# Kernel optimization log

Hardware: AMD Instinct MI355X
Metric: run time of the kernel (lower is better)

## Reference

```python
import jax, jax.numpy as jnp
import numpy as np

WH, WW, WD = 4, 4, 4
NUM_HEADS = 12


def _relative_coords():
    # (3, N) flattened coords of the 3D window, N = WH*WW*WD
    g = jnp.stack(jnp.meshgrid(jnp.arange(WH), jnp.arange(WW), jnp.arange(WD), indexing='ij'), axis=0)
    flat = g.reshape(3, -1)
    rel = flat[:, :, None] - flat[:, None, :]          # (3, N, N)
    return jnp.transpose(rel, (1, 2, 0)).astype(jnp.float32)  # (N, N, 3)


def setup_inputs() -> dict:
    key = jax.random.key(0)
    ks = jax.random.split(key, 9)
    B_, N, C = 2048, WH * WW * WD, 384
    s = lambda fan: 1.0 / np.sqrt(fan)
    return {
        'x': jax.random.normal(ks[0], (B_, N, C), jnp.float32),
        'qkv_w': jax.random.normal(ks[1], (C, 3 * C), jnp.float32) * s(C),
        'qkv_b': jax.random.normal(ks[2], (3 * C,), jnp.float32) * 0.02,
        'proj_w': jax.random.normal(ks[3], (C, C), jnp.float32) * s(C),
        'proj_b': jax.random.normal(ks[4], (C,), jnp.float32) * 0.02,
        'mlp_w1': jax.random.normal(ks[5], (3, 64), jnp.float32) * s(3),
        'mlp_b1': jax.random.normal(ks[6], (64,), jnp.float32) * 0.02,
        'mlp_w2': jax.random.normal(ks[7], (64, NUM_HEADS), jnp.float32) * s(64),
        'mlp_b2': jax.random.normal(ks[8], (NUM_HEADS,), jnp.float32) * 0.02,
    }


def reference(x, qkv_w, qkv_b, proj_w, proj_b, mlp_w1, mlp_b1, mlp_w2, mlp_b2):
    B_, N, C = x.shape
    H = NUM_HEADS
    hd = C // H
    scale = hd ** -0.5

    qkv = (x @ qkv_w + qkv_b).reshape(B_, N, 3, H, hd)
    q, k, v = qkv[:, :, 0], qkv[:, :, 1], qkv[:, :, 2]   # (B_, N, H, hd)

    # MLP-based relative position bias: (N, N, 3) -> (H, N, N)
    rel = _relative_coords()
    bias = jax.nn.relu(rel @ mlp_w1 + mlp_b1) @ mlp_w2 + mlp_b2  # (N, N, H)
    bias = jnp.transpose(bias, (2, 0, 1))                        # (H, N, N)

    attn = jnp.einsum('bnhd,bmhd->bhnm', q, k) * scale + bias[None]
    attn = jax.nn.softmax(attn, axis=-1)

    out = jnp.einsum('bhnm,bmhd->bnhd', attn, v).reshape(B_, N, C)
    return out @ proj_w + proj_b
```

## Files before the change

kernel.cpp:

```cpp
#include <hip/hip_runtime.h>
#include <stdint.h>

#define NTOK 64
#define CDIM 384
#define NH   12
#define HD   32
#define SCALE 0.17677669529663687f

typedef __attribute__((ext_vector_type(8))) short short8;
typedef __attribute__((ext_vector_type(4))) float floatx4;

__device__ __forceinline__ unsigned short f2bf(float f) {
    union { float f; unsigned u; } v; v.f = f;
    unsigned r = (v.u + 0x7fffu + ((v.u >> 16) & 1u)) >> 16;
    return (unsigned short)r;
}

__global__ void prep_weights(const float* __restrict__ qkv_w,
                             const float* __restrict__ proj_w,
                             unsigned short* __restrict__ qkv_wt,
                             unsigned short* __restrict__ proj_wt) {
    int i = blockIdx.x * blockDim.x + threadIdx.x;
    const int nq = 1152 * 384;
    const int np = 384 * 384;
    if (i < nq) {
        int r = i / 384, c = i - r * 384;
        qkv_wt[i] = f2bf(qkv_w[c * 1152 + r]);
    } else if (i < nq + np) {
        int o = i - nq;
        int r = o / 384, c = o - r * 384;
        proj_wt[o] = f2bf(proj_w[c * 384 + r]);
    }
}

__global__ void prep_bias(const float* __restrict__ w1, const float* __restrict__ b1,
                          const float* __restrict__ w2, const float* __restrict__ b2,
                          float* __restrict__ bt) {
    int t = blockIdx.x * blockDim.x + threadIdx.x;
    int i = t >> 6, j = t & 63;
    float r0 = (float)((i >> 4) - (j >> 4));
    float r1 = (float)(((i >> 2) & 3) - ((j >> 2) & 3));
    float r2 = (float)((i & 3) - (j & 3));
    float acc[NH];
#pragma unroll
    for (int h = 0; h < NH; ++h) acc[h] = b2[h];
    for (int u = 0; u < 64; ++u) {
        float hv = r0 * w1[u] + r1 * w1[64 + u] + r2 * w1[128 + u] + b1[u];
        hv = fmaxf(hv, 0.f);
#pragma unroll
        for (int h = 0; h < NH; ++h) acc[h] += hv * w2[u * NH + h];
    }
    for (int h = 0; h < NH; ++h) bt[(h << 12) + (i << 6) + j] = acc[h];
}

#define XP  392
#define QKP 40
#define VTP 72
#define PBP 72

__launch_bounds__(256, 1)
__global__ void win_attn(const float* __restrict__ x,
                         const unsigned short* __restrict__ qkv_wt,
                         const float* __restrict__ qkv_b,
                         const unsigned short* __restrict__ proj_wt,
                         const float* __restrict__ proj_b,
                         const float* __restrict__ bt,
                         float* __restrict__ out) {
    __shared__ unsigned short xs[64 * XP];
    __shared__ unsigned short ao[64 * XP];
    __shared__ unsigned short qls[2][64 * QKP];
    __shared__ unsigned short kls[2][64 * QKP];
    __shared__ unsigned short vts[2][32 * VTP];
    __shared__ unsigned short pbs[2][64 * PBP];
    const int tid  = threadIdx.x;
    const int lane = tid & 63;
    const int w    = tid >> 6;
    const int l15  = lane & 15;
    const int quad = lane >> 4;
    const int b    = blockIdx.x;

    const float* xb = x + (size_t)b * (64 * 384);
    for (int it = 0; it < 24; ++it) {
        int idx = it * 256 + tid;
        int row = idx / 96;
        int c4  = idx - row * 96;
        const float4 v = *reinterpret_cast<const float4*>(xb + row * 384 + c4 * 4);
        uint2 pk;
        pk.x = (unsigned)f2bf(v.x) | ((unsigned)f2bf(v.y) << 16);
        pk.y = (unsigned)f2bf(v.z) | ((unsigned)f2bf(v.w) << 16);
        *reinterpret_cast<uint2*>(&xs[row * XP + c4 * 4]) = pk;
    }
    __syncthreads();

    const int hh = w >> 1;
    const int d2 = w & 1;
    float rs[2][4];
    const floatx4 zf4 = {0.f, 0.f, 0.f, 0.f};

#pragma unroll 1
    for (int hp = 0; hp < 6; ++hp) {
        floatx4 acc[3][4];
#pragma unroll
        for (int j = 0; j < 3; ++j)
#pragma unroll
            for (int m = 0; m < 4; ++m) acc[j][m] = zf4;

        int colbase[3];
#pragma unroll
        for (int j = 0; j < 3; ++j)
            colbase[j] = j * 384 + (2 * hp + hh) * 32 + d2 * 16;

#pragma unroll
        for (int kk = 0; kk < 12; ++kk) {
            short8 a[4];
#pragma unroll
            for (int m = 0; m < 4; ++m)
                a[m] = *reinterpret_cast<const short8*>(
                    &xs[(16 * m + l15) * XP + kk * 32 + quad * 8]);
#pragma unroll
            for (int j = 0; j < 3; ++j) {
                const short8 bf = *reinterpret_cast<const short8*>(
                    qkv_wt + (size_t)(colbase[j] + l15) * 384 + kk * 32 + quad * 8);
#pragma unroll
                for (int m = 0; m < 4; ++m)
                    acc[j][m] = __builtin_amdgcn_mfma_f32_16x16x32_bf16(a[m], bf, acc[j][m], 0, 0, 0);
            }
        }
#pragma unroll
        for (int j = 0; j < 3; ++j) {
            const float bc = qkv_b[colbase[j] + l15];
            if (j < 2) {
                unsigned short* dst = (j == 0) ? qls[hh] : kls[hh];
#pragma unroll
                for (int m = 0; m < 4; ++m)
#pragma unroll
                    for (int r = 0; r < 4; ++r) {
                        int tok = 16 * m + quad * 4 + r;
                        dst[tok * QKP + d2 * 16 + l15] = f2bf(acc[j][m][r] + bc);
                    }
            } else {
#pragma unroll
                for (int m = 0; m < 4; ++m) {
                    uint2 pk;
                    pk.x = (unsigned)f2bf(acc[2][m][0] + bc) | ((unsigned)f2bf(acc[2][m][1] + bc) << 16);
                    pk.y = (unsigned)f2bf(acc[2][m][2] + bc) | ((unsigned)f2bf(acc[2][m][3] + bc) << 16);
                    *reinterpret_cast<uint2*>(
                        &vts[hh][(d2 * 16 + l15) * VTP + 16 * m + quad * 4]) = pk;
                }
            }
        }
        __syncthreads();

#pragma unroll
        for (int hi = 0; hi < 2; ++hi) {
            const int h = 2 * hp + hi;
            const short8 aq = *reinterpret_cast<const short8*>(
                &qls[hi][(16 * w + l15) * QKP + quad * 8]);
            floatx4 s4[4];
#pragma unroll
            for (int c = 0; c < 4; ++c) {
                const short8 bk = *reinterpret_cast<const short8*>(
                    &kls[hi][(16 * c + l15) * QKP + quad * 8]);
                s4[c] = __builtin_amdgcn_mfma_f32_16x16x32_bf16(aq, bk, zf4, 0, 0, 0);
            }
            const float* bth = bt + ((size_t)h << 12);
#pragma unroll
            for (int r = 0; r < 4; ++r) {
                const int n = 16 * w + quad * 4 + r;
#pragma unroll
                for (int c = 0; c < 4; ++c)
                    s4[c][r] = s4[c][r] * SCALE + bth[(n << 6) + 16 * c + l15];
                float m0 = fmaxf(fmaxf(s4[0][r], s4[1][r]), fmaxf(s4[2][r], s4[3][r]));
#pragma unroll
                for (int sh = 1; sh < 16; sh <<= 1) m0 = fmaxf(m0, __shfl_xor(m0, sh, 16));
                float p0 = 0.f;
#pragma unroll
                for (int c = 0; c < 4; ++c) {
                    float p = __expf(s4[c][r] - m0);
                    s4[c][r] = p;
                    p0 += p;
                }
#pragma unroll
                for (int sh = 1; sh < 16; sh <<= 1) p0 += __shfl_xor(p0, sh, 16);
                rs[hi][r] = 1.f / p0;
#pragma unroll
                for (int c = 0; c < 4; ++c)
                    pbs[hi][n * PBP + 16 * c + l15] = f2bf(s4[c][r]);
            }
        }
        __syncthreads();

#pragma unroll
        for (int hi = 0; hi < 2; ++hi) {
            const int h = 2 * hp + hi;
            short8 ap[2];
#pragma unroll
            for (int kk = 0; kk < 2; ++kk)
                ap[kk] = *reinterpret_cast<const short8*>(
                    &pbs[hi][(16 * w + l15) * PBP + kk * 32 + quad * 8]);
#pragma unroll
            for (int t = 0; t < 2; ++t) {
                floatx4 oacc = zf4;
#pragma unroll
                for (int kk = 0; kk < 2; ++kk) {
                    const short8 bv = *reinterpret_cast<const short8*>(
                        &vts[hi][(16 * t + l15) * VTP + kk * 32 + quad * 8]);
                    oacc = __builtin_amdgcn_mfma_f32_16x16x32_bf16(ap[kk], bv, oacc, 0, 0, 0);
                }
#pragma unroll
                for (int r = 0; r < 4; ++r) {
                    int tok = 16 * w + quad * 4 + r;
                    ao[tok * XP + h * 32 + 16 * t + l15] = f2bf(oacc[r] * rs[hi][r]);
                }
            }
        }
        __syncthreads();
    }

    float* ob = out + (size_t)b * (64 * 384);
#pragma unroll 1
    for (int pass = 0; pass < 2; ++pass) {
        const int ntb = pass * 12 + w * 3;
        floatx4 acc2[3][4];
#pragma unroll
        for (int j = 0; j < 3; ++j)
#pragma unroll
            for (int m = 0; m < 4; ++m) acc2[j][m] = zf4;

#pragma unroll
        for (int kk = 0; kk < 12; ++kk) {
            short8 a2[4];
#pragma unroll
            for (int m = 0; m < 4; ++m)
                a2[m] = *reinterpret_cast<const short8*>(
                    &ao[(16 * m + l15) * XP + kk * 32 + quad * 8]);
#pragma unroll
            for (int j = 0; j < 3; ++j) {
                const short8 bf = *reinterpret_cast<const short8*>(
                    proj_wt + (size_t)((ntb + j) * 16 + l15) * 384 + kk * 32 + quad * 8);
#pragma unroll
                for (int m = 0; m < 4; ++m)
                    acc2[j][m] = __builtin_amdgcn_mfma_f32_16x16x32_bf16(a2[m], bf, acc2[j][m], 0, 0, 0);
            }
        }
#pragma unroll
        for (int j = 0; j < 3; ++j) {
            const int col = (ntb + j) * 16 + l15;
            const float pbias = proj_b[col];
#pragma unroll
            for (int m = 0; m < 4; ++m)
#pragma unroll
                for (int r = 0; r < 4; ++r)
                    ob[(16 * m + quad * 4 + r) * 384 + col] = acc2[j][m][r] + pbias;
        }
    }
}

extern "C" void kernel_launch(void* const* d_in, const int* in_sizes, int n_in,
                              void* d_out, int out_size, void* d_ws, size_t ws_size,
                              hipStream_t stream) {
    const float* x      = (const float*)d_in[0];
    const float* qkv_w  = (const float*)d_in[1];
    const float* qkv_b  = (const float*)d_in[2];
    const float* proj_w = (const float*)d_in[3];
    const float* proj_b = (const float*)d_in[4];
    const float* mlp_w1 = (const float*)d_in[5];
    const float* mlp_b1 = (const float*)d_in[6];
    const float* mlp_w2 = (const float*)d_in[7];
    const float* mlp_b2 = (const float*)d_in[8];
    float* out = (float*)d_out;

    unsigned short* qkv_wt  = (unsigned short*)d_ws;
    unsigned short* proj_wt = qkv_wt + 1152 * 384;
    float*          bt      = (float*)(proj_wt + 384 * 384);

    prep_weights<<<2304, 256, 0, stream>>>(qkv_w, proj_w, qkv_wt, proj_wt);
    prep_bias<<<16, 256, 0, stream>>>(mlp_w1, mlp_b1, mlp_w2, mlp_b2, bt);
    win_attn<<<2048, 256, 0, stream>>>(x, qkv_wt, qkv_b, proj_wt, proj_b, bt, out);
}
```

Measured before the change: 874.4 us.

## Double block to 512 threads and split window work across eight waves

Launches the window-attention kernel with 8 wavefronts instead of 4. The QKV GEMM is split by token halves, each wave handles one head's row block in softmax and PV, and the projection is done in one pass. Because each wave only reads back the probability rows it wrote itself, the barrier between softmax and PV is removed. The aim is more latency hiding and fewer barriers, at the cost of halving per-wave MFMA reuse of the global weight fragments. That means more weight loads per block and a tighter register budget under launch_bounds(512,2).

```diff
diff --git a/kernel.cpp b/kernel.cpp
--- a/kernel.cpp
+++ b/kernel.cpp
@@ -58,7 +58,7 @@
 #define VTP 72
 #define PBP 72
 
-__launch_bounds__(256, 1)
+__launch_bounds__(512, 2)
 __global__ void win_attn(const float* __restrict__ x,
                          const unsigned short* __restrict__ qkv_wt,
                          const float* __restrict__ qkv_b,
@@ -80,8 +80,9 @@
     const int b    = blockIdx.x;
 
     const float* xb = x + (size_t)b * (64 * 384);
-    for (int it = 0; it < 24; ++it) {
-        int idx = it * 256 + tid;
+#pragma unroll
+    for (int it = 0; it < 12; ++it) {
+        int idx = it * 512 + tid;
         int row = idx / 96;
         int c4  = idx - row * 96;
         const float4 v = *reinterpret_cast<const float4*>(xb + row * 384 + c4 * 4);
@@ -92,18 +93,22 @@
     }
     __syncthreads();
 
-    const int hh = w >> 1;
-    const int d2 = w & 1;
-    float rs[2][4];
+    const int hh = w & 1;
+    const int d2 = (w >> 1) & 1;
+    const int mh = w >> 2;
+    const int hi = w >> 2;
+    const int rb = w & 3;
+
+    float rs[4];
     const floatx4 zf4 = {0.f, 0.f, 0.f, 0.f};
 
 #pragma unroll 1
     for (int hp = 0; hp < 6; ++hp) {
-        floatx4 acc[3][4];
+        floatx4 acc[3][2];
 #pragma unroll
         for (int j = 0; j < 3; ++j)
 #pragma unroll
-            for (int m = 0; m < 4; ++m) acc[j][m] = zf4;
+            for (int mi = 0; mi < 2; ++mi) acc[j][mi] = zf4;
 
         int colbase[3];
 #pragma unroll
@@ -112,18 +117,18 @@
 
 #pragma unroll
         for (int kk = 0; kk < 12; ++kk) {
-            short8 a[4];
-#pragma unroll
-            for (int m = 0; m < 4; ++m)
-                a[m] = *reinterpret_cast<const short8*>(
-                    &xs[(16 * m + l15) * XP + kk * 32 + quad * 8]);
+            short8 a[2];
+#pragma unroll
+            for (int mi = 0; mi < 2; ++mi)
+                a[mi] = *reinterpret_cast<const short8*>(
+                    &xs[(16 * (2 * mh + mi) + l15) * XP + kk * 32 + quad * 8]);
 #pragma unroll
             for (int j = 0; j < 3; ++j) {
                 const short8 bf = *reinterpret_cast<const short8*>(
                     qkv_wt + (size_t)(colbase[j] + l15) * 384 + kk * 32 + quad * 8);
 #pragma unroll
-                for (int m = 0; m < 4; ++m)
-                    acc[j][m] = __builtin_amdgcn_mfma_f32_16x16x32_bf16(a[m], bf, acc[j][m], 0, 0, 0);
+                for (int mi = 0; mi < 2; ++mi)
+                    acc[j][mi] = __builtin_amdgcn_mfma_f32_16x16x32_bf16(a[mi], bf, acc[j][mi], 0, 0, 0);
             }
         }
 #pragma unroll
@@ -132,30 +137,29 @@
             if (j < 2) {
                 unsigned short* dst = (j == 0) ? qls[hh] : kls[hh];
 #pragma unroll
-                for (int m = 0; m < 4; ++m)
+                for (int mi = 0; mi < 2; ++mi)
 #pragma unroll
                     for (int r = 0; r < 4; ++r) {
-                        int tok = 16 * m + quad * 4 + r;
-                        dst[tok * QKP + d2 * 16 + l15] = f2bf(acc[j][m][r] + bc);
+                        int tok = 16 * (2 * mh + mi) + quad * 4 + r;
+                        dst[tok * QKP + d2 * 16 + l15] = f2bf(acc[j][mi][r] + bc);
                     }
             } else {
 #pragma unroll
-                for (int m = 0; m < 4; ++m) {
+                for (int mi = 0; mi < 2; ++mi) {
                     uint2 pk;
-                    pk.x = (unsigned)f2bf(acc[2][m][0] + bc) | ((unsigned)f2bf(acc[2][m][1] + bc) << 16);
-                    pk.y = (unsigned)f2bf(acc[2][m][2] + bc) | ((unsigned)f2bf(acc[2][m][3] + bc) << 16);
+                    pk.x = (unsigned)f2bf(acc[2][mi][0] + bc) | ((unsigned)f2bf(acc[2][mi][1] + bc) << 16);
+                    pk.y = (unsigned)f2bf(acc[2][mi][2] + bc) | ((unsigned)f2bf(acc[2][mi][3] + bc) << 16);
                     *reinterpret_cast<uint2*>(
-                        &vts[hh][(d2 * 16 + l15) * VTP + 16 * m + quad * 4]) = pk;
+                        &vts[hh][(d2 * 16 + l15) * VTP + 16 * (2 * mh + mi) + quad * 4]) = pk;
                 }
             }
         }
         __syncthreads();
 
-#pragma unroll
-        for (int hi = 0; hi < 2; ++hi) {
+        {
             const int h = 2 * hp + hi;
             const short8 aq = *reinterpret_cast<const short8*>(
-                &qls[hi][(16 * w + l15) * QKP + quad * 8]);
+                &qls[hi][(16 * rb + l15) * QKP + quad * 8]);
             floatx4 s4[4];
 #pragma unroll
             for (int c = 0; c < 4; ++c) {
@@ -166,7 +170,7 @@
             const float* bth = bt + ((size_t)h << 12);
 #pragma unroll
             for (int r = 0; r < 4; ++r) {
-                const int n = 16 * w + quad * 4 + r;
+                const int n = 16 * rb + quad * 4 + r;
 #pragma unroll
                 for (int c = 0; c < 4; ++c)
                     s4[c][r] = s4[c][r] * SCALE + bth[(n << 6) + 16 * c + l15];
@@ -182,22 +186,20 @@
                 }
 #pragma unroll
                 for (int sh = 1; sh < 16; sh <<= 1) p0 += __shfl_xor(p0, sh, 16);
-                rs[hi][r] = 1.f / p0;
+                rs[r] = 1.f / p0;
 #pragma unroll
                 for (int c = 0; c < 4; ++c)
                     pbs[hi][n * PBP + 16 * c + l15] = f2bf(s4[c][r]);
             }
         }
-        __syncthreads();
-
-#pragma unroll
-        for (int hi = 0; hi < 2; ++hi) {
+
+        {
             const int h = 2 * hp + hi;
             short8 ap[2];
 #pragma unroll
             for (int kk = 0; kk < 2; ++kk)
                 ap[kk] = *reinterpret_cast<const short8*>(
-                    &pbs[hi][(16 * w + l15) * PBP + kk * 32 + quad * 8]);
+                    &pbs[hi][(16 * rb + l15) * PBP + kk * 32 + quad * 8]);
 #pragma unroll
             for (int t = 0; t < 2; ++t) {
                 floatx4 oacc = zf4;
@@ -209,8 +211,8 @@
                 }
 #pragma unroll
                 for (int r = 0; r < 4; ++r) {
-                    int tok = 16 * w + quad * 4 + r;
-                    ao[tok * XP + h * 32 + 16 * t + l15] = f2bf(oacc[r] * rs[hi][r]);
+                    int tok = 16 * rb + quad * 4 + r;
+                    ao[tok * XP + h * 32 + 16 * t + l15] = f2bf(oacc[r] * rs[r]);
                 }
             }
         }
@@ -218,9 +220,8 @@
     }
 
     float* ob = out + (size_t)b * (64 * 384);
-#pragma unroll 1
-    for (int pass = 0; pass < 2; ++pass) {
-        const int ntb = pass * 12 + w * 3;
+    {
+        const int ntb = w * 3;
         floatx4 acc2[3][4];
 #pragma unroll
         for (int j = 0; j < 3; ++j)
@@ -276,5 +277,5 @@
 
     prep_weights<<<2304, 256, 0, stream>>>(qkv_w, proj_w, qkv_wt, proj_wt);
     prep_bias<<<16, 256, 0, stream>>>(mlp_w1, mlp_b1, mlp_w2, mlp_b2, bt);
-    win_attn<<<2048, 256, 0, stream>>>(x, qkv_wt, qkv_b, proj_wt, proj_b, bt, out);
-}
+    win_attn<<<2048, 512, 0, stream>>>(x, qkv_wt, qkv_b, proj_wt, proj_b, bt, out);
+}
```

Measured after the change: 918.3 us. 5.0% more time.

## Restructure window attention to 6 waves, per-head loop, fused incremental projection

Applied to the files above, without the earlier changes.

The block grows to 384 threads (6 waves) and processes one head per iteration instead of head pairs: each wave computes one 16-column slice of q, k or v. The attention output for that head goes into a small per-head LDS tile and is immediately accumulated into the output projection in registers, which removes the full 64x384 attention-output LDS buffer. Shared memory drops roughly by half, targeting 3 blocks per CU. The trade-off is more barriers per head, idle waves during softmax (only 4 of 6 active), and a larger persistent register accumulator.

```diff
diff --git a/kernel.cpp b/kernel.cpp
--- a/kernel.cpp
+++ b/kernel.cpp
@@ -1,10 +1,6 @@
 #include <hip/hip_runtime.h>
 #include <stdint.h>
 
-#define NTOK 64
-#define CDIM 384
-#define NH   12
-#define HD   32
 #define SCALE 0.17677669529663687f
 
 typedef __attribute__((ext_vector_type(8))) short short8;
@@ -41,24 +37,25 @@
     float r0 = (float)((i >> 4) - (j >> 4));
     float r1 = (float)(((i >> 2) & 3) - ((j >> 2) & 3));
     float r2 = (float)((i & 3) - (j & 3));
-    float acc[NH];
-#pragma unroll
-    for (int h = 0; h < NH; ++h) acc[h] = b2[h];
+    float acc[12];
+#pragma unroll
+    for (int h = 0; h < 12; ++h) acc[h] = b2[h];
     for (int u = 0; u < 64; ++u) {
         float hv = r0 * w1[u] + r1 * w1[64 + u] + r2 * w1[128 + u] + b1[u];
         hv = fmaxf(hv, 0.f);
 #pragma unroll
-        for (int h = 0; h < NH; ++h) acc[h] += hv * w2[u * NH + h];
-    }
-    for (int h = 0; h < NH; ++h) bt[(h << 12) + (i << 6) + j] = acc[h];
+        for (int h = 0; h < 12; ++h) acc[h] += hv * w2[u * 12 + h];
+    }
+    for (int h = 0; h < 12; ++h) bt[(h << 12) + (i << 6) + j] = acc[h];
 }
 
 #define XP  392
 #define QKP 40
 #define VTP 72
 #define PBP 72
-
-__launch_bounds__(256, 1)
+#define OSP 40
+
+__launch_bounds__(384, 3)
 __global__ void win_attn(const float* __restrict__ x,
                          const unsigned short* __restrict__ qkv_wt,
                          const float* __restrict__ qkv_b,
@@ -67,11 +64,11 @@
                          const float* __restrict__ bt,
                          float* __restrict__ out) {
     __shared__ unsigned short xs[64 * XP];
-    __shared__ unsigned short ao[64 * XP];
-    __shared__ unsigned short qls[2][64 * QKP];
-    __shared__ unsigned short kls[2][64 * QKP];
-    __shared__ unsigned short vts[2][32 * VTP];
-    __shared__ unsigned short pbs[2][64 * PBP];
+    __shared__ unsigned short ql[64 * QKP];
+    __shared__ unsigned short kl[64 * QKP];
+    __shared__ unsigned short vt[32 * VTP];
+    __shared__ unsigned short pb[64 * PBP];
+    __shared__ unsigned short osl[64 * OSP];
     const int tid  = threadIdx.x;
     const int lane = tid & 63;
     const int w    = tid >> 6;
@@ -80,8 +77,9 @@
     const int b    = blockIdx.x;
 
     const float* xb = x + (size_t)b * (64 * 384);
-    for (int it = 0; it < 24; ++it) {
-        int idx = it * 256 + tid;
+#pragma unroll
+    for (int it = 0; it < 16; ++it) {
+        int idx = it * 384 + tid;
         int row = idx / 96;
         int c4  = idx - row * 96;
         const float4 v = *reinterpret_cast<const float4*>(xb + row * 384 + c4 * 4);
@@ -92,75 +90,68 @@
     }
     __syncthreads();
 
-    const int hh = w >> 1;
+    const int j3 = w >> 1;
     const int d2 = w & 1;
-    float rs[2][4];
     const floatx4 zf4 = {0.f, 0.f, 0.f, 0.f};
 
+    floatx4 acc2[4][4];
+#pragma unroll
+    for (int jj = 0; jj < 4; ++jj)
+#pragma unroll
+        for (int m = 0; m < 4; ++m) acc2[jj][m] = zf4;
+
+    float rs[4];
+
 #pragma unroll 1
-    for (int hp = 0; hp < 6; ++hp) {
-        floatx4 acc[3][4];
-#pragma unroll
-        for (int j = 0; j < 3; ++j)
-#pragma unroll
-            for (int m = 0; m < 4; ++m) acc[j][m] = zf4;
-
-        int colbase[3];
-#pragma unroll
-        for (int j = 0; j < 3; ++j)
-            colbase[j] = j * 384 + (2 * hp + hh) * 32 + d2 * 16;
+    for (int h = 0; h < 12; ++h) {
+        floatx4 acc[4];
+#pragma unroll
+        for (int m = 0; m < 4; ++m) acc[m] = zf4;
+        const int colbase = j3 * 384 + h * 32 + d2 * 16;
+        const unsigned short* wcol = qkv_wt + (size_t)(colbase + l15) * 384;
 
 #pragma unroll
         for (int kk = 0; kk < 12; ++kk) {
+            const short8 bf = *reinterpret_cast<const short8*>(wcol + kk * 32 + quad * 8);
             short8 a[4];
 #pragma unroll
             for (int m = 0; m < 4; ++m)
                 a[m] = *reinterpret_cast<const short8*>(
                     &xs[(16 * m + l15) * XP + kk * 32 + quad * 8]);
 #pragma unroll
-            for (int j = 0; j < 3; ++j) {
-                const short8 bf = *reinterpret_cast<const short8*>(
-                    qkv_wt + (size_t)(colbase[j] + l15) * 384 + kk * 32 + quad * 8);
+            for (int m = 0; m < 4; ++m)
+                acc[m] = __builtin_amdgcn_mfma_f32_16x16x32_bf16(a[m], bf, acc[m], 0, 0, 0);
+        }
+        {
+            const float bc = qkv_b[colbase + l15];
+            if (j3 < 2) {
+                unsigned short* dst = (j3 == 0) ? ql : kl;
 #pragma unroll
                 for (int m = 0; m < 4; ++m)
-                    acc[j][m] = __builtin_amdgcn_mfma_f32_16x16x32_bf16(a[m], bf, acc[j][m], 0, 0, 0);
-            }
-        }
-#pragma unroll
-        for (int j = 0; j < 3; ++j) {
-            const float bc = qkv_b[colbase[j] + l15];
-            if (j < 2) {
-                unsigned short* dst = (j == 0) ? qls[hh] : kls[hh];
-#pragma unroll
-                for (int m = 0; m < 4; ++m)
-#pragma unroll
-                    for (int r = 0; r < 4; ++r) {
-                        int tok = 16 * m + quad * 4 + r;
-                        dst[tok * QKP + d2 * 16 + l15] = f2bf(acc[j][m][r] + bc);
-                    }
+#pragma unroll
+                    for (int r = 0; r < 4; ++r)
+                        dst[(16 * m + quad * 4 + r) * QKP + d2 * 16 + l15] = f2bf(acc[m][r] + bc);
             } else {
 #pragma unroll
                 for (int m = 0; m < 4; ++m) {
                     uint2 pk;
-                    pk.x = (unsigned)f2bf(acc[2][m][0] + bc) | ((unsigned)f2bf(acc[2][m][1] + bc) << 16);
-                    pk.y = (unsigned)f2bf(acc[2][m][2] + bc) | ((unsigned)f2bf(acc[2][m][3] + bc) << 16);
+                    pk.x = (unsigned)f2bf(acc[m][0] + bc) | ((unsigned)f2bf(acc[m][1] + bc) << 16);
+                    pk.y = (unsigned)f2bf(acc[m][2] + bc) | ((unsigned)f2bf(acc[m][3] + bc) << 16);
                     *reinterpret_cast<uint2*>(
-                        &vts[hh][(d2 * 16 + l15) * VTP + 16 * m + quad * 4]) = pk;
+                        &vt[(d2 * 16 + l15) * VTP + 16 * m + quad * 4]) = pk;
                 }
             }
         }
         __syncthreads();
 
-#pragma unroll
-        for (int hi = 0; hi < 2; ++hi) {
-            const int h = 2 * hp + hi;
+        if (w < 4) {
             const short8 aq = *reinterpret_cast<const short8*>(
-                &qls[hi][(16 * w + l15) * QKP + quad * 8]);
+                &ql[(16 * w + l15) * QKP + quad * 8]);
             floatx4 s4[4];
 #pragma unroll
             for (int c = 0; c < 4; ++c) {
                 const short8 bk = *reinterpret_cast<const short8*>(
-                    &kls[hi][(16 * c + l15) * QKP + quad * 8]);
+                    &kl[(16 * c + l15) * QKP + quad * 8]);
                 s4[c] = __builtin_amdgcn_mfma_f32_16x16x32_bf16(aq, bk, zf4, 0, 0, 0);
             }
             const float* bth = bt + ((size_t)h << 12);
@@ -182,77 +173,59 @@
                 }
 #pragma unroll
                 for (int sh = 1; sh < 16; sh <<= 1) p0 += __shfl_xor(p0, sh, 16);
-                rs[hi][r] = 1.f / p0;
+                rs[r] = 1.f / p0;
 #pragma unroll
                 for (int c = 0; c < 4; ++c)
-                    pbs[hi][n * PBP + 16 * c + l15] = f2bf(s4[c][r]);
-            }
-        }
-        __syncthreads();
-
-#pragma unroll
-        for (int hi = 0; hi < 2; ++hi) {
-            const int h = 2 * hp + hi;
+                    pb[n * PBP + 16 * c + l15] = f2bf(s4[c][r]);
+            }
             short8 ap[2];
 #pragma unroll
-            for (int kk = 0; kk < 2; ++kk)
-                ap[kk] = *reinterpret_cast<const short8*>(
-                    &pbs[hi][(16 * w + l15) * PBP + kk * 32 + quad * 8]);
+            for (int kkp = 0; kkp < 2; ++kkp)
+                ap[kkp] = *reinterpret_cast<const short8*>(
+                    &pb[(16 * w + l15) * PBP + kkp * 32 + quad * 8]);
 #pragma unroll
             for (int t = 0; t < 2; ++t) {
                 floatx4 oacc = zf4;
 #pragma unroll
-                for (int kk = 0; kk < 2; ++kk) {
+                for (int kkp = 0; kkp < 2; ++kkp) {
                     const short8 bv = *reinterpret_cast<const short8*>(
-                        &vts[hi][(16 * t + l15) * VTP + kk * 32 + quad * 8]);
-                    oacc = __builtin_amdgcn_mfma_f32_16x16x32_bf16(ap[kk], bv, oacc, 0, 0, 0);
+                        &vt[(16 * t + l15) * VTP + kkp * 32 + quad * 8]);
+                    oacc = __builtin_amdgcn_mfma_f32_16x16x32_bf16(ap[kkp], bv, oacc, 0, 0, 0);
                 }
 #pragma unroll
-                for (int r = 0; r < 4; ++r) {
-                    int tok = 16 * w + quad * 4 + r;
-                    ao[tok * XP + h * 32 + 16 * t + l15] = f2bf(oacc[r] * rs[hi][r]);
-                }
+                for (int r = 0; r < 4; ++r)
+                    osl[(16 * w + quad * 4 + r) * OSP + 16 * t + l15] = f2bf(oacc[r] * rs[r]);
             }
         }
         __syncthreads();
-    }
-
-    float* ob = out + (size_t)b * (64 * 384);
-#pragma unroll 1
-    for (int pass = 0; pass < 2; ++pass) {
-        const int ntb = pass * 12 + w * 3;
-        floatx4 acc2[3][4];
-#pragma unroll
-        for (int j = 0; j < 3; ++j)
-#pragma unroll
-            for (int m = 0; m < 4; ++m) acc2[j][m] = zf4;
-
-#pragma unroll
-        for (int kk = 0; kk < 12; ++kk) {
+
+        {
             short8 a2[4];
 #pragma unroll
             for (int m = 0; m < 4; ++m)
                 a2[m] = *reinterpret_cast<const short8*>(
-                    &ao[(16 * m + l15) * XP + kk * 32 + quad * 8]);
-#pragma unroll
-            for (int j = 0; j < 3; ++j) {
-                const short8 bf = *reinterpret_cast<const short8*>(
-                    proj_wt + (size_t)((ntb + j) * 16 + l15) * 384 + kk * 32 + quad * 8);
+                    &osl[(16 * m + l15) * OSP + quad * 8]);
+#pragma unroll
+            for (int jj = 0; jj < 4; ++jj) {
+                const short8 b2 = *reinterpret_cast<const short8*>(
+                    proj_wt + (size_t)((w * 4 + jj) * 16 + l15) * 384 + h * 32 + quad * 8);
 #pragma unroll
                 for (int m = 0; m < 4; ++m)
-                    acc2[j][m] = __builtin_amdgcn_mfma_f32_16x16x32_bf16(a2[m], bf, acc2[j][m], 0, 0, 0);
-            }
-        }
-#pragma unroll
-        for (int j = 0; j < 3; ++j) {
-            const int col = (ntb + j) * 16 + l15;
-            const float pbias = proj_b[col];
-#pragma unroll
-            for (int m = 0; m < 4; ++m)
-#pragma unroll
-                for (int r = 0; r < 4; ++r)
-                    ob[(16 * m + quad * 4 + r) * 384 + col] = acc2[j][m][r] + pbias;
-        }
+                    acc2[jj][m] = __builtin_amdgcn_mfma_f32_16x16x32_bf16(a2[m], b2, acc2[jj][m], 0, 0, 0);
+            }
+        }
+    }
+
+    float* ob = out + (size_t)b * (64 * 384);
+#pragma unroll
+    for (int jj = 0; jj < 4; ++jj) {
+        const int col = (w * 4 + jj) * 16 + l15;
+        const float pbias = proj_b[col];
+#pragma unroll
+        for (int m = 0; m < 4; ++m)
+#pragma unroll
+            for (int r = 0; r < 4; ++r)
+                ob[(16 * m + quad * 4 + r) * 384 + col] = acc2[jj][m][r] + pbias;
     }
 }
 
@@ -276,5 +249,5 @@
 
     prep_weights<<<2304, 256, 0, stream>>>(qkv_w, proj_w, qkv_wt, proj_wt);
     prep_bias<<<16, 256, 0, stream>>>(mlp_w1, mlp_b1, mlp_w2, mlp_b2, bt);
-    win_attn<<<2048, 256, 0, stream>>>(x, qkv_wt, qkv_b, proj_wt, proj_b, bt, out);
-}
+    win_attn<<<2048, 384, 0, stream>>>(x, qkv_wt, qkv_b, proj_wt, proj_b, bt, out);
+}
```

Result: faster. 844.5 us (-3.4%).
